# Optimization experiments

Hardware: AMD Instinct MI355X
Metric: run time of the kernel (lower is better)

The kernel has to match this reference:

```python
import jax, jax.numpy as jnp
import numpy as np

# NSA hyperparams (match init_kwargs)
D_BLK = 64    # d: block stride
L_CMP = 64    # compression block length (== d -> non-overlapping blocks)
L_SLC = 64    # selection block length (== l_cmp == d -> P_slc = P_cmp)
BQ = 64       # block_size_q
TOPK = 16     # slc_top_k
WL, WR = 512, 0  # sliding window (left, right)


def _nsa_forward(q, k, v, w_k, b_k, w_v, b_v, w_gate, b_gate, seqlen):
    S, qh, dim = q.shape
    kv = k.shape[1]
    H = qh // kv
    b = S // seqlen          # number of equal-length packed sequences
    s = seqlen
    scale = dim ** -0.5
    f32 = jnp.float32

    # [b, s, kv, H, e]: q head g*H+h belongs to kv head g (repeat_interleave layout)
    q5 = q.reshape(b, s, kv, H, dim)
    k3 = k.reshape(b, s, kv, dim)
    v3 = v.reshape(b, s, kv, dim)

    # ---- block compression (extract_blocks + cmp_linear over block length) ----
    n_blk = s // D_BLK
    kb = k.reshape(b, n_blk, D_BLK, kv, dim)
    vb = v.reshape(b, n_blk, D_BLK, kv, dim)
    K_cmp = jnp.einsum('bntke,t->bnke', kb, w_k) + b_k[0]
    V_cmp = jnp.einsum('bntke,t->bnke', vb, w_v) + b_v[0]

    # ---- compressed attention (per sequence, fp32 softmax) ----
    sc = jnp.einsum('bqkhe,bnke->bkhqn', q5, K_cmp).astype(f32) * scale
    P = jax.nn.softmax(sc, axis=-1)
    out_cmp = jnp.einsum('bkhqn,bnke->bqkhe', P.astype(q.dtype), V_cmp)

    # ---- selection scores: pool P over q-blocks and GQA groups, then top-k ----
    nqb = s // BQ
    pooled = P.reshape(b, kv, H, nqb, BQ, n_blk).sum(axis=(2, 4))  # [b,kv,nqb,n_blk]
    idx = jax.lax.top_k(pooled, TOPK)[1]                            # [b,kv,nqb,TOPK]

    # gather selected K/V blocks (shared by all queries in a q-block / GQA group)
    kb2 = jnp.transpose(kb, (0, 3, 1, 2, 4))  # [b,kv,n_blk,l,e]
    vb2 = jnp.transpose(vb, (0, 3, 1, 2, 4))
    gather = jax.vmap(jax.vmap(lambda blocks, i: blocks[i]))
    K_sel = gather(kb2, idx)  # [b,kv,nqb,TOPK,l,e]
    V_sel = gather(vb2, idx)

    # ---- selected-block attention ----
    qblk = q5.reshape(b, nqb, BQ, kv, H, dim)
    sc2 = jnp.einsum('bnckhe,bkntle->bkhnctl', qblk, K_sel).astype(f32) * scale
    sc2 = sc2.reshape(b, kv, H, nqb, BQ, TOPK * L_SLC)
    P2 = jax.nn.softmax(sc2, axis=-1).astype(q.dtype)
    out_slc = jnp.einsum('bkhncm,bknme->bnckhe', P2,
                         V_sel.reshape(b, kv, nqb, TOPK * L_SLC, dim))
    out_slc = out_slc.reshape(b, s, kv, H, dim)

    # ---- sliding-window attention (window_size=(WL, WR), non-causal flag) ----
    sw = jnp.einsum('bikhe,bjke->bkhij', q5, k3).astype(f32) * scale
    i = jnp.arange(s)[:, None]
    j = jnp.arange(s)[None, :]
    valid = (j >= i - WL) & (j <= i + WR)
    sw = jnp.where(valid, sw, -jnp.inf)
    Pw = jax.nn.softmax(sw, axis=-1).astype(q.dtype)
    out_win = jnp.einsum('bkhij,bjke->bikhe', Pw, v3)

    # ---- gated fusion of the three branches ----
    gate = jax.nn.sigmoid(jnp.einsum('bqkhe,ec->bqkhc', q5, w_gate) + b_gate)
    out = (gate[..., 0:1] * out_cmp
           + gate[..., 1:2] * out_slc
           + gate[..., 2:3] * out_win)
    return out.reshape(S, qh, dim)


def setup_inputs() -> dict:
    key = jax.random.key(0)
    ks = jax.random.split(key, 9)
    S, qh, kvh, dim = 4096, 8, 2, 128
    inp = {
        'q': jax.random.normal(ks[0], (S, qh, dim), jnp.float32),
        'k': jax.random.normal(ks[1], (S, kvh, dim), jnp.float32),
        'v': jax.random.normal(ks[2], (S, kvh, dim), jnp.float32),
        'w_k': jax.random.normal(ks[3], (L_CMP,), jnp.float32) * (L_CMP ** -0.5),
        'b_k': jax.random.normal(ks[4], (1,), jnp.float32) * 0.02,
        'w_v': jax.random.normal(ks[5], (L_CMP,), jnp.float32) * (L_CMP ** -0.5),
        'b_v': jax.random.normal(ks[6], (1,), jnp.float32) * 0.02,
        'w_gate': jax.random.normal(ks[7], (dim, 3), jnp.float32) * (dim ** -0.5),
        'b_gate': jax.random.normal(ks[8], (3,), jnp.float32) * 0.02,
        'seqlen': 2048,
    }
    return inp


def reference(q, k, v, w_k, b_k, w_v, b_v, w_gate, b_gate, seqlen):
    return _nsa_forward(q, k, v, w_k, b_k, w_v, b_v, w_gate, b_gate, seqlen)
```

## Files before the change

kernel.cpp:

```cpp
#include <hip/hip_runtime.h>
#include <hip/hip_bf16.h>


#define SEQ   2048
#define NB    2
#define KV    2
#define NH    4
#define QH    8
#define DIM   128
#define NBLK  32
#define NQB   32
#define NTOP  16
#define SCALE 0.08838834764831845f
#define QSC   0.12751831795244785f
#define QS    36
#define RS    144
#define VP    72

typedef unsigned short ushort_t;
using bf16x8 = __attribute__((ext_vector_type(8))) short;
using f32x4  = __attribute__((ext_vector_type(4))) float;

__device__ __forceinline__ unsigned pkbf(float a, float b){
  union { __hip_bfloat162 h; unsigned u; } cv;
  cv.h = __float22bfloat162_rn(make_float2(a, b));
  return cv.u;
}

__device__ __forceinline__ void async16(ushort_t* l, const ushort_t* g){
  __builtin_amdgcn_global_load_lds(
      (const __attribute__((address_space(1))) unsigned int*)(size_t)g,
      (__attribute__((address_space(3))) unsigned int*)(size_t)l,
      16, 0, 0);
}

__global__ __launch_bounds__(256) void prep_k(
    const float* __restrict__ k, const float* __restrict__ v,
    ushort_t* __restrict__ Kb, ushort_t* __restrict__ VT)
{
  int blk = blockIdx.x;
  int db = blk & 1, rb = (blk >> 1) & 31, bbg = blk >> 6;
  int bb = bbg >> 1, g = bbg & 1;
  int tid = threadIdx.x;
  __shared__ ushort_t T[64*VP];

  for (int jj = 0; jj < 4; ++jj){
    int i = tid + jj*256;
    int r = i >> 4, ds = i & 15;
    size_t src = ((size_t)(bb*SEQ + rb*64 + r)*KV + g)*DIM + db*64 + ds*4;
    float4 kx = *(const float4*)(k + src);
    float4 vx = *(const float4*)(v + src);
    uint2 kk; kk.x = pkbf(kx.x,kx.y); kk.y = pkbf(kx.z,kx.w);
    size_t rowb = ((size_t)bbg*SEQ + rb*64 + r)*DIM*2;
    int swz = (db*128 + ds*8) ^ ((r & 7) << 4);
    *(uint2*)((char*)Kb + rowb + swz) = kk;
    unsigned v01 = pkbf(vx.x,vx.y), v23 = pkbf(vx.z,vx.w);
    T[(ds*4+0)*VP + r] = (ushort_t)(v01 & 0xffffu);
    T[(ds*4+1)*VP + r] = (ushort_t)(v01 >> 16);
    T[(ds*4+2)*VP + r] = (ushort_t)(v23 & 0xffffu);
    T[(ds*4+3)*VP + r] = (ushort_t)(v23 >> 16);
  }
  __syncthreads();
  for (int jj = 0; jj < 4; ++jj){
    int i = tid + jj*256;
    int d = i >> 4, seg = i & 15;
    uint2 u = *(uint2*)&T[d*VP + seg*4];
    size_t rowb = ((size_t)bbg*DIM + db*64 + d)*SEQ*2;
    int swz = (seg*8) ^ ((d & 7) << 4);
    *(uint2*)((char*)VT + rowb + rb*128 + swz) = u;
  }
}

__global__ __launch_bounds__(256) void compress_k(
    const float* __restrict__ k, const float* __restrict__ v,
    const float* __restrict__ w_k, const float* __restrict__ b_k,
    const float* __restrict__ w_v, const float* __restrict__ b_v,
    float* __restrict__ Kc, float* __restrict__ Vc)
{
  int blk = blockIdx.x;
  int dh = blk & 1;
  int n  = (blk >> 1) & 31;
  int g  = (blk >> 6) & 1;
  int bb = blk >> 7;
  int tid = threadIdx.x;

  __shared__ float wks[64], wvs[64];
  __shared__ float accK[16][64], accV[16][64];
  if (tid < 64){ wks[tid] = w_k[tid]; wvs[tid] = w_v[tid]; }
  __syncthreads();

  int r4 = tid >> 4, dq = tid & 15;
  float4 sk = {0,0,0,0}, sv = {0,0,0,0};
  for (int rr = 0; rr < 4; ++rr){
    int row = r4*4 + rr;
    size_t off = ((size_t)(bb*SEQ + n*64 + row)*KV + g)*DIM + dh*64 + dq*4;
    float4 kx = *(const float4*)(k + off);
    float4 vx = *(const float4*)(v + off);
    float a = wks[row], b = wvs[row];
    sk.x += a*kx.x; sk.y += a*kx.y; sk.z += a*kx.z; sk.w += a*kx.w;
    sv.x += b*vx.x; sv.y += b*vx.y; sv.z += b*vx.z; sv.w += b*vx.w;
  }
  *(float4*)&accK[r4][dq*4] = sk;
  *(float4*)&accV[r4][dq*4] = sv;
  __syncthreads();
  size_t obase = ((size_t)((bb*KV+g)*NBLK + n))*DIM + dh*64;
  if (tid < 64){
    float s = 0.f;
#pragma unroll
    for (int i = 0; i < 16; ++i) s += accK[i][tid];
    Kc[obase + tid] = s + b_k[0];
  } else if (tid < 128){
    int d = tid - 64;
    float s = 0.f;
#pragma unroll
    for (int i = 0; i < 16; ++i) s += accV[i][d];
    Vc[obase + d] = s + b_v[0];
  }
}

__global__ __launch_bounds__(256) void cmp_attn_k(
    const float* __restrict__ q, const float* __restrict__ Kc,
    const float* __restrict__ Vc,
    const float* __restrict__ w_gate, const float* __restrict__ b_gate,
    float* __restrict__ pooled_part, float* __restrict__ out)
{
  int blk = blockIdx.x;
  int h  = blk & 3;
  int qb = (blk >> 2) & (NQB-1);
  int g  = (blk >> 7) & 1;
  int bb = blk >> 8;
  int tid = threadIdx.x;
  int qi = tid >> 2, c = tid & 3;

  __shared__ float Ks[32*RS];
  __shared__ float Vs[32*RS];
  __shared__ float wsum[4][NBLK];

  const float4* Ksrc = (const float4*)(Kc + (size_t)(bb*KV + g) * NBLK * DIM);
  const float4* Vsrc = (const float4*)(Vc + (size_t)(bb*KV + g) * NBLK * DIM);
  for (int i = tid; i < 1024; i += 256){
    int row = i >> 5, seg = i & 31;
    int dst = row*RS + (seg>>3)*QS + (seg&7)*4;
    ((float4*)(Ks+dst))[0] = Ksrc[i];
    ((float4*)(Vs+dst))[0] = Vsrc[i];
  }
  __syncthreads();

  int row = bb*SEQ + qb*64 + qi;
  float qv[32];
  {
    const float4* q4 = (const float4*)(q + ((size_t)row*QH + g*NH + h)*DIM + c*32);
#pragma unroll
    for (int j = 0; j < 8; ++j){
      float4 u = q4[j];
      qv[4*j+0]=u.x; qv[4*j+1]=u.y; qv[4*j+2]=u.z; qv[4*j+3]=u.w;
    }
  }

  float gp = 0.f;
#pragma unroll
  for (int d = 0; d < 32; ++d) gp += qv[d]*w_gate[(c*32+d)*3 + 0];
  gp += __shfl_xor(gp, 1); gp += __shfl_xor(gp, 2);
  float g0 = 1.f/(1.f + expf(-(gp + b_gate[0])));

  float sc[NBLK];
#pragma unroll
  for (int n = 0; n < NBLK; ++n){
    float p = 0.f;
    const float4* kr = (const float4*)(Ks + n*RS + c*QS);
#pragma unroll
    for (int j = 0; j < 8; ++j){
      float4 u = kr[j];
      p += qv[4*j+0]*u.x + qv[4*j+1]*u.y + qv[4*j+2]*u.z + qv[4*j+3]*u.w;
    }
    p += __shfl_xor(p, 1); p += __shfl_xor(p, 2);
    sc[n] = p * SCALE;
  }
  float m = sc[0];
#pragma unroll
  for (int n = 1; n < NBLK; ++n) m = fmaxf(m, sc[n]);
  float l = 0.f;
#pragma unroll
  for (int n = 0; n < NBLK; ++n){ sc[n] = expf(sc[n]-m); l += sc[n]; }
  float inv = 1.f/l;
#pragma unroll
  for (int n = 0; n < NBLK; ++n) sc[n] *= inv;

#pragma unroll
  for (int n = 0; n < NBLK; ++n){
    float t2 = sc[n];
    t2 += __shfl_xor(t2, 4); t2 += __shfl_xor(t2, 8);
    t2 += __shfl_xor(t2, 16); t2 += __shfl_xor(t2, 32);
    if ((tid & 63) == 0) wsum[tid>>6][n] = t2;
  }
  __syncthreads();
  if (tid < NBLK)
    pooled_part[(size_t)blk*NBLK + tid] =
        (wsum[0][tid]+wsum[1][tid]) + (wsum[2][tid]+wsum[3][tid]);

  float o[32];
#pragma unroll
  for (int d = 0; d < 32; ++d) o[d] = 0.f;
#pragma unroll
  for (int n = 0; n < NBLK; ++n){
    float pb = sc[n];
    const float4* vr = (const float4*)(Vs + n*RS + c*QS);
#pragma unroll
    for (int j = 0; j < 8; ++j){
      float4 u = vr[j];
      o[4*j+0] += pb*u.x; o[4*j+1] += pb*u.y;
      o[4*j+2] += pb*u.z; o[4*j+3] += pb*u.w;
    }
  }
  float* op = out + ((size_t)row*QH + g*NH + h)*DIM + c*32;
#pragma unroll
  for (int d = 0; d < 32; ++d) op[d] = g0*o[d];
}

__global__ __launch_bounds__(512, 2) void attn_k(
    const float* __restrict__ q, const ushort_t* __restrict__ Kb,
    const ushort_t* __restrict__ VT, const float* __restrict__ pp,
    const float* __restrict__ w_gate, const float* __restrict__ b_gate,
    float* __restrict__ slcbuf, float* __restrict__ out)
{
  int idx = blockIdx.x;
  int x = idx & 7, low = idx & 1, u = idx >> 3;
  int bbg = x >> 1;
  int j = u*2 + low;
  int role = j >> 5;
  int qb = j & 31;
  int bb = bbg >> 1, g = bbg & 1;

  int tid = threadIdx.x;
  int lane = tid & 63, w = tid >> 6;
  int quad = lane >> 4, l15 = lane & 15;
  int h = w & 3, qh2 = w >> 2;
  int xr = (l15 & 7) << 4;

  __shared__ ushort_t Ks[2][64*128];
  __shared__ ushort_t VTs[2][128*64];
  __shared__ ushort_t Ps[256*VP];
  __shared__ float gbuf[256];
  __shared__ int   idxs[NTOP];

  if (role == 0 && tid < 64){
    int n = lane;
    float val = -INFINITY;
    if (n < NBLK){
      const float* p0 = pp + ((size_t)((bb*KV+g)*NQB + qb)*NH)*NBLK + n;
      val = (p0[0] + p0[NBLK]) + (p0[2*NBLK] + p0[3*NBLK]);
    }
    for (int t = 0; t < NTOP; ++t){
      float bv = val; int bi = n;
      for (int mm = 1; mm < 32; mm <<= 1){
        float ov = __shfl_xor(bv, mm);
        int   oi = __shfl_xor(bi, mm);
        if (ov > bv || (ov == bv && oi < bi)){ bv = ov; bi = oi; }
      }
      if (lane == 0) idxs[t] = bi;
      if (n == bi) val = -INFINITY;
    }
  }

  const float* qrow0 = q + ((size_t)(bb*SEQ + qb*64 + qh2*32 + l15)*QH + g*NH + h)*DIM;
  const float* qrow1 = qrow0 + (size_t)16*QH*DIM;
  int gcol = 1 + role;
  bf16x8 qfrag0[4], qfrag1[4];
  float gp0 = 0.f, gp1 = 0.f;
#pragma unroll
  for (int kc = 0; kc < 4; ++kc){
    int d0 = kc*32 + quad*8;
    float4 a0 = *(const float4*)(qrow0 + d0);
    float4 a1 = *(const float4*)(qrow0 + d0 + 4);
    float4 b0 = *(const float4*)(qrow1 + d0);
    float4 b1 = *(const float4*)(qrow1 + d0 + 4);
    float qa[8] = {a0.x,a0.y,a0.z,a0.w,a1.x,a1.y,a1.z,a1.w};
    float qc[8] = {b0.x,b0.y,b0.z,b0.w,b1.x,b1.y,b1.z,b1.w};
#pragma unroll
    for (int jj = 0; jj < 8; ++jj){
      float wg = w_gate[(d0+jj)*3 + gcol];
      gp0 += qa[jj]*wg; gp1 += qc[jj]*wg;
    }
    union { unsigned uu[4]; bf16x8 v8; } t0, t1;
#pragma unroll
    for (int p2 = 0; p2 < 4; ++p2){
      t0.uu[p2] = pkbf(qa[2*p2]*QSC, qa[2*p2+1]*QSC);
      t1.uu[p2] = pkbf(qc[2*p2]*QSC, qc[2*p2+1]*QSC);
    }
    qfrag0[kc] = t0.v8; qfrag1[kc] = t1.v8;
  }
  gp0 += __shfl_xor(gp0,16); gp0 += __shfl_xor(gp0,32);
  gp1 += __shfl_xor(gp1,16); gp1 += __shfl_xor(gp1,32);
  if (quad == 0){
    gbuf[w*32 + l15]      = 1.f/(1.f + __expf(-(gp0 + b_gate[gcol])));
    gbuf[w*32 + 16 + l15] = 1.f/(1.f + __expf(-(gp1 + b_gate[gcol])));
  }
  __syncthreads();
  float gl0[4], gl1[4];
#pragma unroll
  for (int r = 0; r < 4; ++r){
    gl0[r] = gbuf[w*32 + quad*4 + r];
    gl1[r] = gbuf[w*32 + 16 + quad*4 + r];
  }

  const ushort_t* kbase  = Kb + (size_t)bbg*SEQ*DIM;
  const ushort_t* vtbase = VT + (size_t)bbg*DIM*SEQ;

  int kb0 = (qb >= 8) ? (qb - 8) : 0;
  int nph = (role == 0) ? NTOP : (qb - kb0 + 1);
  int qi0 = qh2*32 + l15, qi1 = qi0 + 16;

  float m10 = -INFINITY, l10 = 0.f, m11 = -INFINITY, l11 = 0.f;
  f32x4 oacc0[8], oacc1[8];
  const f32x4 zero4 = {0.f,0.f,0.f,0.f};
#pragma unroll
  for (int dt = 0; dt < 8; ++dt){ oacc0[dt] = zero4; oacc1[dt] = zero4; }

  auto stage = [&](int bufi, int kb_){
    const ushort_t* ksrc = kbase + (size_t)kb_*64*DIM;
#pragma unroll
    for (int jj = 0; jj < 2; ++jj)
      async16(&Ks[bufi][(jj*512 + w*64)*8], ksrc + (size_t)(tid + jj*512)*8);
    const ushort_t* vsrc = vtbase + kb_*64;
#pragma unroll
    for (int jj = 0; jj < 2; ++jj){
      int i = tid + jj*512;
      int d = i >> 3, sg = i & 7;
      async16(&VTs[bufi][(jj*512 + w*64)*8], vsrc + (size_t)d*SEQ + sg*8);
    }
  };

  stage(0, (role == 0) ? idxs[0] : kb0);

  for (int t = 0; t < nph; ++t){
    int cur = t & 1;
    int kb = (role == 0) ? idxs[t] : (kb0 + t);
    __syncthreads();
    if (t+1 < nph){
      int kbn = (role == 0) ? idxs[t+1] : (kb0 + t + 1);
      stage(cur ^ 1, kbn);
    }
    __builtin_amdgcn_sched_barrier(0);

    f32x4 sacc0[4], sacc1[4];
#pragma unroll
    for (int nt = 0; nt < 4; ++nt){ sacc0[nt] = zero4; sacc1[nt] = zero4; }
    __builtin_amdgcn_s_setprio(1);
#pragma unroll
    for (int kc = 0; kc < 4; ++kc){
#pragma unroll
      for (int nt = 0; nt < 4; ++nt){
        bf16x8 a = *(bf16x8*)((char*)&Ks[cur][0] + (nt*16 + l15)*256
                              + ((kc*64 + quad*16) ^ xr));
        sacc0[nt] = __builtin_amdgcn_mfma_f32_16x16x32_bf16(a, qfrag0[kc], sacc0[nt], 0, 0, 0);
        sacc1[nt] = __builtin_amdgcn_mfma_f32_16x16x32_bf16(a, qfrag1[kc], sacc1[nt], 0, 0, 0);
      }
    }
    __builtin_amdgcn_s_setprio(0);

    bool mlow  = (role == 1) && (kb == qb - 8);
    bool mhigh = (role == 1) && (kb == qb);
    bool domask = mlow | mhigh;

    auto softmax_qt = [&](f32x4* sc, float& m1r, float& l1r, int qi_l,
                          bool& skipped) -> float {
      float mx = -INFINITY;
      if (domask){
#pragma unroll
        for (int nt = 0; nt < 4; ++nt)
#pragma unroll
          for (int r = 0; r < 4; ++r){
            int key = nt*16 + quad*4 + r;
            float sv = sc[nt][r];
            bool valid = (!mlow || key >= qi_l) && (!mhigh || key <= qi_l);
            sv = valid ? sv : -INFINITY;
            sc[nt][r] = sv;
            mx = fmaxf(mx, sv);
          }
      } else {
#pragma unroll
        for (int nt = 0; nt < 4; ++nt)
#pragma unroll
          for (int r = 0; r < 4; ++r) mx = fmaxf(mx, sc[nt][r]);
      }
      mx = fmaxf(mx, __shfl_xor(mx, 16));
      mx = fmaxf(mx, __shfl_xor(mx, 32));
      float al = 1.f;
      skipped = __all(mx <= m1r + 8.f);
      if (!skipped){
        float mn = fmaxf(m1r, mx);
        al = exp2f(m1r - mn);
        m1r = mn;
      }
      float s0 = 0.f;
#pragma unroll
      for (int nt = 0; nt < 4; ++nt)
#pragma unroll
        for (int r = 0; r < 4; ++r){
          float pe = exp2f(sc[nt][r] - m1r);
          sc[nt][r] = pe;
          s0 += pe;
        }
      s0 += __shfl_xor(s0, 16);
      s0 += __shfl_xor(s0, 32);
      l1r = l1r*al + s0;
      return al;
    };
    bool sk0, sk1;
    float al0 = softmax_qt(sacc0, m10, l10, qi0, sk0);
    float al1 = softmax_qt(sacc1, m11, l11, qi1, sk1);

#pragma unroll
    for (int nt = 0; nt < 4; ++nt){
      uint2 p0, p1;
      p0.x = pkbf(sacc0[nt][0], sacc0[nt][1]);
      p0.y = pkbf(sacc0[nt][2], sacc0[nt][3]);
      p1.x = pkbf(sacc1[nt][0], sacc1[nt][1]);
      p1.y = pkbf(sacc1[nt][2], sacc1[nt][3]);
      *(uint2*)&Ps[(w*32 + l15)*VP + nt*16 + quad*4] = p0;
      *(uint2*)&Ps[(w*32 + 16 + l15)*VP + nt*16 + quad*4] = p1;
    }

    if (!sk0){
      float ar[4];
#pragma unroll
      for (int r = 0; r < 4; ++r) ar[r] = __shfl(al0, quad*4 + r);
#pragma unroll
      for (int dt = 0; dt < 8; ++dt)
#pragma unroll
        for (int r = 0; r < 4; ++r) oacc0[dt][r] *= ar[r];
    }
    if (!sk1){
      float ar[4];
#pragma unroll
      for (int r = 0; r < 4; ++r) ar[r] = __shfl(al1, quad*4 + r);
#pragma unroll
      for (int dt = 0; dt < 8; ++dt)
#pragma unroll
        for (int r = 0; r < 4; ++r) oacc1[dt][r] *= ar[r];
    }

#pragma unroll
    for (int kc2 = 0; kc2 < 2; ++kc2){
      bf16x8 pa0 = *(bf16x8*)&Ps[(w*32 + l15)*VP + kc2*32 + quad*8];
      bf16x8 pa1 = *(bf16x8*)&Ps[(w*32 + 16 + l15)*VP + kc2*32 + quad*8];
      __builtin_amdgcn_s_setprio(1);
#pragma unroll
      for (int dt = 0; dt < 8; ++dt){
        bf16x8 vb8 = *(bf16x8*)((char*)&VTs[cur][0] + (dt*16 + l15)*128
                                + ((kc2*64 + quad*16) ^ xr));
        oacc0[dt] = __builtin_amdgcn_mfma_f32_16x16x32_bf16(pa0, vb8, oacc0[dt], 0, 0, 0);
        oacc1[dt] = __builtin_amdgcn_mfma_f32_16x16x32_bf16(pa1, vb8, oacc1[dt], 0, 0, 0);
      }
      __builtin_amdgcn_s_setprio(0);
    }
  }

  float lr0[4], lr1[4];
#pragma unroll
  for (int r = 0; r < 4; ++r){
    lr0[r] = __shfl(l10, quad*4 + r);
    lr1[r] = __shfl(l11, quad*4 + r);
  }
#pragma unroll
  for (int r = 0; r < 4; ++r){
    float s20 = gl0[r] / lr0[r];
    float s21 = gl1[r] / lr1[r];
    size_t ob0 = ((size_t)(bb*SEQ + qb*64 + qh2*32 + quad*4 + r)*QH + g*NH + h)*DIM + l15;
    size_t ob1 = ob0 + (size_t)16*QH*DIM;
    if (role == 0){
      float* op0 = slcbuf + ob0;
      float* op1 = slcbuf + ob1;
#pragma unroll
      for (int dt = 0; dt < 8; ++dt){
        op0[dt*16] = s20 * oacc0[dt][r];
        op1[dt*16] = s21 * oacc1[dt][r];
      }
    } else {
      float* op0 = out + ob0;
      float* op1 = out + ob1;
#pragma unroll
      for (int dt = 0; dt < 8; ++dt){
        op0[dt*16] += s20 * oacc0[dt][r];
        op1[dt*16] += s21 * oacc1[dt][r];
      }
    }
  }
}

__global__ __launch_bounds__(256) void merge_k(const float* __restrict__ slcbuf,
                                               float* __restrict__ out){
  int i = blockIdx.x * 256 + threadIdx.x;
  float4 a = ((const float4*)slcbuf)[i];
  float4 b = ((float4*)out)[i];
  b.x += a.x; b.y += a.y; b.z += a.z; b.w += a.w;
  ((float4*)out)[i] = b;
}

extern "C" void kernel_launch(void* const* d_in, const int* in_sizes, int n_in,
                              void* d_out, int out_size, void* d_ws, size_t ws_size,
                              hipStream_t stream) {
  const float* q      = (const float*)d_in[0];
  const float* k      = (const float*)d_in[1];
  const float* v      = (const float*)d_in[2];
  const float* w_k    = (const float*)d_in[3];
  const float* b_k    = (const float*)d_in[4];
  const float* w_v    = (const float*)d_in[5];
  const float* b_v    = (const float*)d_in[6];
  const float* w_gate = (const float*)d_in[7];
  const float* b_gate = (const float*)d_in[8];
  float* out = (float*)d_out;

  float* ws     = (float*)d_ws;
  float* Kc     = ws;
  float* Vc     = ws + 16384;
  float* pp     = ws + 32768;
  float* slcbuf = ws + 49152;
  ushort_t* Kb  = (ushort_t*)(ws + 4243456);
  ushort_t* VT  = Kb + 1048576;

  prep_k    <<<256, 256, 0, stream>>>(k, v, Kb, VT);
  compress_k<<<256, 256, 0, stream>>>(k, v, w_k, b_k, w_v, b_v, Kc, Vc);
  cmp_attn_k<<<NB*KV*NQB*NH, 256, 0, stream>>>(q, Kc, Vc, w_gate, b_gate, pp, out);
  attn_k    <<<256, 512, 0, stream>>>(q, Kb, VT, pp, w_gate, b_gate, slcbuf, out);
  merge_k   <<<4096, 256, 0, stream>>>(slcbuf, out);
}
```

Baseline: 186.0 us.

## Fuse block compression into prep kernel and restructure compressed-attention score split

New measurement: 178.6 us. -4.0%, faster.

```diff
diff --git a/kernel.cpp b/kernel.cpp
--- a/kernel.cpp
+++ b/kernel.cpp
@@ -15,6 +15,7 @@
 #define QSC   0.12751831795244785f
 #define QS    36
 #define RS    144
+#define PLS   33
 #define VP    72
 
 typedef unsigned short ushort_t;
@@ -36,14 +37,23 @@
 
 __global__ __launch_bounds__(256) void prep_k(
     const float* __restrict__ k, const float* __restrict__ v,
-    ushort_t* __restrict__ Kb, ushort_t* __restrict__ VT)
+    const float* __restrict__ w_k, const float* __restrict__ b_k,
+    const float* __restrict__ w_v, const float* __restrict__ b_v,
+    ushort_t* __restrict__ Kb, ushort_t* __restrict__ VT,
+    float* __restrict__ Kc, float* __restrict__ Vc)
 {
   int blk = blockIdx.x;
   int db = blk & 1, rb = (blk >> 1) & 31, bbg = blk >> 6;
   int bb = bbg >> 1, g = bbg & 1;
   int tid = threadIdx.x;
   __shared__ ushort_t T[64*VP];
-
+  __shared__ float wks[64], wvs[64];
+  __shared__ float accK[16][64], accV[16][64];
+
+  if (tid < 64){ wks[tid] = w_k[tid]; wvs[tid] = w_v[tid]; }
+  __syncthreads();
+
+  float4 sk = {0,0,0,0}, sv = {0,0,0,0};
   for (int jj = 0; jj < 4; ++jj){
     int i = tid + jj*256;
     int r = i >> 4, ds = i & 15;
@@ -59,8 +69,14 @@
     T[(ds*4+1)*VP + r] = (ushort_t)(v01 >> 16);
     T[(ds*4+2)*VP + r] = (ushort_t)(v23 & 0xffffu);
     T[(ds*4+3)*VP + r] = (ushort_t)(v23 >> 16);
-  }
+    float a = wks[r], b = wvs[r];
+    sk.x += a*kx.x; sk.y += a*kx.y; sk.z += a*kx.z; sk.w += a*kx.w;
+    sv.x += b*vx.x; sv.y += b*vx.y; sv.z += b*vx.z; sv.w += b*vx.w;
+  }
+  *(float4*)&accK[tid>>4][(tid&15)*4] = sk;
+  *(float4*)&accV[tid>>4][(tid&15)*4] = sv;
   __syncthreads();
+
   for (int jj = 0; jj < 4; ++jj){
     int i = tid + jj*256;
     int d = i >> 4, seg = i & 15;
@@ -69,41 +85,8 @@
     int swz = (seg*8) ^ ((d & 7) << 4);
     *(uint2*)((char*)VT + rowb + rb*128 + swz) = u;
   }
-}
-
-__global__ __launch_bounds__(256) void compress_k(
-    const float* __restrict__ k, const float* __restrict__ v,
-    const float* __restrict__ w_k, const float* __restrict__ b_k,
-    const float* __restrict__ w_v, const float* __restrict__ b_v,
-    float* __restrict__ Kc, float* __restrict__ Vc)
-{
-  int blk = blockIdx.x;
-  int dh = blk & 1;
-  int n  = (blk >> 1) & 31;
-  int g  = (blk >> 6) & 1;
-  int bb = blk >> 7;
-  int tid = threadIdx.x;
-
-  __shared__ float wks[64], wvs[64];
-  __shared__ float accK[16][64], accV[16][64];
-  if (tid < 64){ wks[tid] = w_k[tid]; wvs[tid] = w_v[tid]; }
-  __syncthreads();
-
-  int r4 = tid >> 4, dq = tid & 15;
-  float4 sk = {0,0,0,0}, sv = {0,0,0,0};
-  for (int rr = 0; rr < 4; ++rr){
-    int row = r4*4 + rr;
-    size_t off = ((size_t)(bb*SEQ + n*64 + row)*KV + g)*DIM + dh*64 + dq*4;
-    float4 kx = *(const float4*)(k + off);
-    float4 vx = *(const float4*)(v + off);
-    float a = wks[row], b = wvs[row];
-    sk.x += a*kx.x; sk.y += a*kx.y; sk.z += a*kx.z; sk.w += a*kx.w;
-    sv.x += b*vx.x; sv.y += b*vx.y; sv.z += b*vx.z; sv.w += b*vx.w;
-  }
-  *(float4*)&accK[r4][dq*4] = sk;
-  *(float4*)&accV[r4][dq*4] = sv;
-  __syncthreads();
-  size_t obase = ((size_t)((bb*KV+g)*NBLK + n))*DIM + dh*64;
+
+  size_t obase = ((size_t)(bbg*NBLK + rb))*DIM + db*64;
   if (tid < 64){
     float s = 0.f;
 #pragma unroll
@@ -134,7 +117,7 @@
 
   __shared__ float Ks[32*RS];
   __shared__ float Vs[32*RS];
-  __shared__ float wsum[4][NBLK];
+  __shared__ float Pl[64*PLS];
 
   const float4* Ksrc = (const float4*)(Kc + (size_t)(bb*KV + g) * NBLK * DIM);
   const float4* Vsrc = (const float4*)(Vc + (size_t)(bb*KV + g) * NBLK * DIM);
@@ -147,63 +130,63 @@
   __syncthreads();
 
   int row = bb*SEQ + qb*64 + qi;
-  float qv[32];
-  {
-    const float4* q4 = (const float4*)(q + ((size_t)row*QH + g*NH + h)*DIM + c*32);
+  const float* qptr = q + ((size_t)row*QH + g*NH + h)*DIM;
+
+  float sc[8];
+#pragma unroll
+  for (int nn = 0; nn < 8; ++nn) sc[nn] = 0.f;
+  float gp = 0.f;
+  for (int qq = 0; qq < 4; ++qq){
+    float qv[32];
+    const float4* q4 = (const float4*)(qptr + qq*32);
 #pragma unroll
     for (int j = 0; j < 8; ++j){
       float4 u = q4[j];
       qv[4*j+0]=u.x; qv[4*j+1]=u.y; qv[4*j+2]=u.z; qv[4*j+3]=u.w;
     }
-  }
-
-  float gp = 0.f;
-#pragma unroll
-  for (int d = 0; d < 32; ++d) gp += qv[d]*w_gate[(c*32+d)*3 + 0];
-  gp += __shfl_xor(gp, 1); gp += __shfl_xor(gp, 2);
+#pragma unroll
+    for (int d = 0; d < 32; ++d) gp += qv[d]*w_gate[(qq*32+d)*3 + 0];
+#pragma unroll
+    for (int nn = 0; nn < 8; ++nn){
+      int n = nn*4 + c;
+      const float4* kr = (const float4*)(Ks + n*RS + qq*QS);
+      float p = 0.f;
+#pragma unroll
+      for (int j = 0; j < 8; ++j){
+        float4 u = kr[j];
+        p += qv[4*j+0]*u.x + qv[4*j+1]*u.y + qv[4*j+2]*u.z + qv[4*j+3]*u.w;
+      }
+      sc[nn] += p;
+    }
+  }
   float g0 = 1.f/(1.f + expf(-(gp + b_gate[0])));
 
-  float sc[NBLK];
-#pragma unroll
+#pragma unroll
+  for (int nn = 0; nn < 8; ++nn) sc[nn] *= SCALE;
+  float m = sc[0];
+#pragma unroll
+  for (int nn = 1; nn < 8; ++nn) m = fmaxf(m, sc[nn]);
+  m = fmaxf(m, __shfl_xor(m, 1)); m = fmaxf(m, __shfl_xor(m, 2));
+  float l = 0.f;
+#pragma unroll
+  for (int nn = 0; nn < 8; ++nn){ sc[nn] = expf(sc[nn]-m); l += sc[nn]; }
+  l += __shfl_xor(l, 1); l += __shfl_xor(l, 2);
+  float inv = 1.f/l;
+#pragma unroll
+  for (int nn = 0; nn < 8; ++nn) Pl[qi*PLS + nn*4 + c] = sc[nn]*inv;
+  __syncthreads();
+
+  if (tid < NBLK){
+    float s = 0.f;
+    for (int q2 = 0; q2 < 64; ++q2) s += Pl[q2*PLS + tid];
+    pooled_part[(size_t)blk*NBLK + tid] = s;
+  }
+
+  float o[32];
+#pragma unroll
+  for (int d = 0; d < 32; ++d) o[d] = 0.f;
   for (int n = 0; n < NBLK; ++n){
-    float p = 0.f;
-    const float4* kr = (const float4*)(Ks + n*RS + c*QS);
-#pragma unroll
-    for (int j = 0; j < 8; ++j){
-      float4 u = kr[j];
-      p += qv[4*j+0]*u.x + qv[4*j+1]*u.y + qv[4*j+2]*u.z + qv[4*j+3]*u.w;
-    }
-    p += __shfl_xor(p, 1); p += __shfl_xor(p, 2);
-    sc[n] = p * SCALE;
-  }
-  float m = sc[0];
-#pragma unroll
-  for (int n = 1; n < NBLK; ++n) m = fmaxf(m, sc[n]);
-  float l = 0.f;
-#pragma unroll
-  for (int n = 0; n < NBLK; ++n){ sc[n] = expf(sc[n]-m); l += sc[n]; }
-  float inv = 1.f/l;
-#pragma unroll
-  for (int n = 0; n < NBLK; ++n) sc[n] *= inv;
-
-#pragma unroll
-  for (int n = 0; n < NBLK; ++n){
-    float t2 = sc[n];
-    t2 += __shfl_xor(t2, 4); t2 += __shfl_xor(t2, 8);
-    t2 += __shfl_xor(t2, 16); t2 += __shfl_xor(t2, 32);
-    if ((tid & 63) == 0) wsum[tid>>6][n] = t2;
-  }
-  __syncthreads();
-  if (tid < NBLK)
-    pooled_part[(size_t)blk*NBLK + tid] =
-        (wsum[0][tid]+wsum[1][tid]) + (wsum[2][tid]+wsum[3][tid]);
-
-  float o[32];
-#pragma unroll
-  for (int d = 0; d < 32; ++d) o[d] = 0.f;
-#pragma unroll
-  for (int n = 0; n < NBLK; ++n){
-    float pb = sc[n];
+    float pb = Pl[qi*PLS + n];
     const float4* vr = (const float4*)(Vs + n*RS + c*QS);
 #pragma unroll
     for (int j = 0; j < 8; ++j){
@@ -519,8 +502,7 @@
   ushort_t* Kb  = (ushort_t*)(ws + 4243456);
   ushort_t* VT  = Kb + 1048576;
 
-  prep_k    <<<256, 256, 0, stream>>>(k, v, Kb, VT);
-  compress_k<<<256, 256, 0, stream>>>(k, v, w_k, b_k, w_v, b_v, Kc, Vc);
+  prep_k    <<<256, 256, 0, stream>>>(k, v, w_k, b_k, w_v, b_v, Kb, VT, Kc, Vc);
   cmp_attn_k<<<NB*KV*NQB*NH, 256, 0, stream>>>(q, Kc, Vc, w_gate, b_gate, pp, out);
   attn_k    <<<256, 512, 0, stream>>>(q, Kb, VT, pp, w_gate, b_gate, slcbuf, out);
   merge_k   <<<4096, 256, 0, stream>>>(slcbuf, out);
```
